# Performance work log

Hardware: AMD Instinct MI355X
Metric: run time of the kernel (lower is better)

The kernel has to match this reference:

```python
import jax, jax.numpy as jnp
import numpy as np

ALPHA = 0.2          # LeakyReLU negative slope
NEG_INF = -9e15      # mask value used by the original module


def setup_inputs() -> dict:
    key = jax.random.key(0)
    k1, k2, k3, k4 = jax.random.split(key, 4)
    N, C, F, H, E = 4096, 512, 64, 8, 131072
    x = jax.random.normal(k1, (N, C), dtype=jnp.float32)
    edge_index = jax.random.randint(k2, (2, E), 0, N, dtype=jnp.int64)
    # xavier_uniform with gain=1.414 (per-head params stacked on leading axis)
    lim_W = 1.414 * np.sqrt(6.0 / (C + F))
    lim_a = 1.414 * np.sqrt(6.0 / (2 * F + 1))
    W = jax.random.uniform(k3, (H, C, F), minval=-lim_W, maxval=lim_W, dtype=jnp.float32)
    a = jax.random.uniform(k4, (H, 2 * F, 1), minval=-lim_a, maxval=lim_a, dtype=jnp.float32)
    return {"x": x, "edge_index": edge_index, "W": W, "a": a}


def reference(x, edge_index, W, a):
    # x: [N, C]; edge_index: [2, E]; W: [H, C, F]; a: [H, 2F, 1]
    N = x.shape[0]
    H, C, F = W.shape
    # dense adjacency with self-loops (duplicate edges collapse to True, matching adj > 0)
    adj = jnp.zeros((N, N), dtype=bool).at[edge_index[0], edge_index[1]].set(True)
    diag = jnp.arange(N)
    adj = adj.at[diag, diag].set(True)
    # per-head projection: h[h_, i] = x_i @ W[h_]
    h = jnp.einsum('nc,hcf->hnf', x, W)                       # [H, N, F]
    # e_ij = leakyrelu(h_i . a[:F] + h_j . a[F:]) -- identical math to the
    # original's NxN pairwise concat, without materializing [N*N, 2F]
    a_src = a[:, :F, 0]                                        # [H, F]
    a_dst = a[:, F:, 0]                                        # [H, F]
    s_src = jnp.einsum('hnf,hf->hn', h, a_src)                 # [H, N]
    s_dst = jnp.einsum('hnf,hf->hn', h, a_dst)                 # [H, N]
    e = s_src[:, :, None] + s_dst[:, None, :]                  # [H, N, N]
    e = jnp.where(e > 0, e, ALPHA * e)                         # LeakyReLU
    e = jnp.where(adj[None, :, :], e, NEG_INF)                 # mask non-edges
    att = jax.nn.softmax(e, axis=-1)                           # row softmax (dropout=0 / eval)
    out = jnp.einsum('hij,hjf->hif', att, h)                   # [H, N, F]
    out = jnp.transpose(out, (1, 0, 2)).reshape(N, H * F)      # concat heads
    return jax.nn.softmax(out, axis=1)
```

## Files before the change

### kernel.cpp

```cpp
#include <hip/hip_runtime.h>

#define ALPHA 0.2f

typedef __attribute__((ext_vector_type(8))) short short8;
typedef __attribute__((ext_vector_type(8))) unsigned short ushort8;
typedef __attribute__((ext_vector_type(4))) float f32x4;

__device__ __forceinline__ float bf2f(unsigned short u) {
    return __uint_as_float(((unsigned int)u) << 16);
}
__device__ __forceinline__ unsigned short f2bf(float f) {
    unsigned int x = __float_as_uint(f);
    unsigned int r = (x + 0x7fffu + ((x >> 16) & 1u)) >> 16;
    return (unsigned short)r;
}

__global__ __launch_bounds__(256) void detect_types(const unsigned int* __restrict__ xw,
                                                    const int* __restrict__ ei32,
                                                    int* __restrict__ flags) {
    __shared__ int cnt[2];
    if (threadIdx.x == 0) { cnt[0] = 0; cnt[1] = 0; }
    __syncthreads();
    int c0 = 0, c1 = 0;
    int t = threadIdx.x;
    for (int i = 0; i < 8; i++) {
        int k = t * 8 + i;
        unsigned int u = xw[k];
        unsigned int e = (u >> 7) & 0xffu;
        if (e >= 0x58u && e <= 0x90u) c0++;
        if (ei32[2 * k + 1] != 0) c1++;
    }
    atomicAdd(&cnt[0], c0);
    atomicAdd(&cnt[1], c1);
    __syncthreads();
    if (threadIdx.x == 0) {
        flags[0] = (cnt[0] < 1200) ? 1 : 0;
        flags[1] = (cnt[1] < 1000) ? 1 : 0;
    }
}

__global__ __launch_bounds__(256) void split_bf16(const void* __restrict__ x_raw,
                                                  const void* __restrict__ W_raw,
                                                  unsigned short* __restrict__ x_hi,
                                                  unsigned short* __restrict__ x_lo,
                                                  unsigned short* __restrict__ wt_hi,
                                                  unsigned short* __restrict__ wt_lo,
                                                  const int* __restrict__ flags) {
    int is32 = flags[0];
    int bid = blockIdx.x, tid = threadIdx.x;
    if (bid < 1024) {
        size_t base = ((size_t)bid * 256 + tid) * 8;
        ushort8 h8, l8;
        if (is32) {
            const float* xf = (const float*)x_raw;
            float4 v0 = *(const float4*)(xf + base);
            float4 v1 = *(const float4*)(xf + base + 4);
            float v[8] = {v0.x, v0.y, v0.z, v0.w, v1.x, v1.y, v1.z, v1.w};
#pragma unroll
            for (int j = 0; j < 8; j++) {
                unsigned short hi = f2bf(v[j]);
                h8[j] = hi;
                l8[j] = f2bf(v[j] - bf2f(hi));
            }
        } else {
            const ushort8* xb = (const ushort8*)x_raw;
            h8 = xb[base / 8];
            l8 = (ushort8)0;
        }
        *(ushort8*)(x_hi + base) = h8;
        *(ushort8*)(x_lo + base) = l8;
    } else {
        size_t u = ((size_t)(bid - 1024) * 256 + tid) * 8;
#pragma unroll
        for (int j = 0; j < 8; j++) {
            size_t e = u + j;
            int head = (int)(e >> 15);
            int c = (int)((e >> 6) & 511);
            int f = (int)(e & 63);
            unsigned short hi, lo;
            if (is32) {
                float v = ((const float*)W_raw)[e];
                hi = f2bf(v);
                lo = f2bf(v - bf2f(hi));
            } else {
                hi = ((const unsigned short*)W_raw)[e];
                lo = 0;
            }
            size_t o = (size_t)head * 32768 + (size_t)f * 512 + c;
            wt_hi[o] = hi;
            wt_lo[o] = lo;
        }
    }
}

__global__ __launch_bounds__(256) void build_adj(const int* __restrict__ ei, int E, int N,
                                                 unsigned long long* __restrict__ adj,
                                                 const int* __restrict__ flags) {
    int is64 = flags[1];
    int t = blockIdx.x * blockDim.x + threadIdx.x;
    int words = N >> 6;
    if (t < E) {
        int r = is64 ? ei[2 * t]       : ei[t];
        int c = is64 ? ei[2 * (E + t)] : ei[E + t];
        atomicOr(&adj[(size_t)r * words + (c >> 6)], 1ull << (c & 63));
    } else if (t < E + N) {
        int i = t - E;
        atomicOr(&adj[(size_t)i * words + (i >> 6)], 1ull << (i & 63));
    }
}

#define LROW 40
__global__ __launch_bounds__(256) void gemm_mfma(const unsigned short* __restrict__ xh,
                                                 const unsigned short* __restrict__ xl,
                                                 const unsigned short* __restrict__ wth,
                                                 const unsigned short* __restrict__ wtl,
                                                 const void* __restrict__ a_raw,
                                                 unsigned short* __restrict__ h2b,
                                                 float* __restrict__ s_src2,
                                                 float* __restrict__ s_dst2,
                                                 const int* __restrict__ flags) {
    __shared__ unsigned short sA[64 * LROW];
    __shared__ unsigned short sB[64 * LROW];

    int head = blockIdx.y;
    int row0 = blockIdx.x * 64;
    int tid = threadIdx.x;
    int w = tid >> 6, lane = tid & 63;
    int m = lane & 15, quad = lane >> 4;
    int sr = tid >> 2, sc = tid & 3;

    const unsigned short* Ap[3] = {xh, xl, xh};
    const unsigned short* Bp[3] = {wth, wth, wtl};
    size_t baseA = (size_t)(row0 + sr) * 512 + sc * 8;
    size_t baseB = (size_t)head * 32768 + (size_t)sr * 512 + sc * 8;

    f32x4 acc[4] = {f32x4{0.f, 0.f, 0.f, 0.f}, f32x4{0.f, 0.f, 0.f, 0.f},
                    f32x4{0.f, 0.f, 0.f, 0.f}, f32x4{0.f, 0.f, 0.f, 0.f}};

    int ldsw = sr * LROW + sc * 8;
    int ldsA = (w * 16 + m) * LROW + quad * 8;

    ushort8 ra0 = *(const ushort8*)(Ap[0] + baseA);
    ushort8 rb0 = *(const ushort8*)(Bp[0] + baseB);
    ushort8 ra1 = *(const ushort8*)(Ap[0] + baseA + 32);
    ushort8 rb1 = *(const ushort8*)(Bp[0] + baseB + 32);

    for (int i = 0; i < 48; i += 2) {
        __syncthreads();
        *(ushort8*)&sA[ldsw] = ra0;
        *(ushort8*)&sB[ldsw] = rb0;
        __syncthreads();
        {
            int inx = i + 2;
            if (inx < 48) {
                int pn = inx >> 4, kn = (inx & 15) * 32;
                ra0 = *(const ushort8*)(Ap[pn] + baseA + kn);
                rb0 = *(const ushort8*)(Bp[pn] + baseB + kn);
            }
        }
        {
            short8 af = *(const short8*)&sA[ldsA];
#pragma unroll
            for (int t = 0; t < 4; t++) {
                short8 bf = *(const short8*)&sB[(t * 16 + m) * LROW + quad * 8];
                acc[t] = __builtin_amdgcn_mfma_f32_16x16x32_bf16(af, bf, acc[t], 0, 0, 0);
            }
        }
        __syncthreads();
        *(ushort8*)&sA[ldsw] = ra1;
        *(ushort8*)&sB[ldsw] = rb1;
        __syncthreads();
        {
            int inx = i + 3;
            if (inx < 48) {
                int pn = inx >> 4, kn = (inx & 15) * 32;
                ra1 = *(const ushort8*)(Ap[pn] + baseA + kn);
                rb1 = *(const ushort8*)(Bp[pn] + baseB + kn);
            }
        }
        {
            short8 af = *(const short8*)&sA[ldsA];
#pragma unroll
            for (int t = 0; t < 4; t++) {
                short8 bf = *(const short8*)&sB[(t * 16 + m) * LROW + quad * 8];
                acc[t] = __builtin_amdgcn_mfma_f32_16x16x32_bf16(af, bf, acc[t], 0, 0, 0);
            }
        }
    }

#pragma unroll
    for (int t = 0; t < 4; t++)
#pragma unroll
        for (int reg = 0; reg < 4; reg++) {
            int r = row0 + w * 16 + quad * 4 + reg;
            h2b[(size_t)r * 512 + head * 64 + t * 16 + m] = f2bf(acc[t][reg]);
        }

    float as[4], ad[4];
    if (flags[0]) {
        const float* af32 = (const float*)a_raw + head * 128;
#pragma unroll
        for (int t = 0; t < 4; t++) {
            as[t] = af32[t * 16 + m];
            ad[t] = af32[64 + t * 16 + m];
        }
    } else {
        const unsigned short* ab = (const unsigned short*)a_raw + head * 128;
#pragma unroll
        for (int t = 0; t < 4; t++) {
            as[t] = bf2f(ab[t * 16 + m]);
            ad[t] = bf2f(ab[64 + t * 16 + m]);
        }
    }
#pragma unroll
    for (int reg = 0; reg < 4; reg++) {
        float s1 = as[0] * acc[0][reg] + as[1] * acc[1][reg] + as[2] * acc[2][reg] + as[3] * acc[3][reg];
        float s2 = ad[0] * acc[0][reg] + ad[1] * acc[1][reg] + ad[2] * acc[2][reg] + ad[3] * acc[3][reg];
#pragma unroll
        for (int d = 1; d < 16; d <<= 1) {
            s1 += __shfl_xor(s1, d);
            s2 += __shfl_xor(s2, d);
        }
        if (m == 0) {
            int r = row0 + w * 16 + quad * 4 + reg;
            s_src2[(size_t)r * 8 + head] = s1;
            s_dst2[(size_t)r * 8 + head] = s2;
        }
    }
}

__global__ __launch_bounds__(256) void attn_out(const unsigned short* __restrict__ h2b,
                                                const float* __restrict__ s_src2,
                                                const float* __restrict__ s_dst2,
                                                const unsigned long long* __restrict__ adj,
                                                void* __restrict__ out_raw,
                                                const int* __restrict__ flags) {
    __shared__ unsigned short nbrs[4096];
    __shared__ float w_lds[256 * 8];
    __shared__ float sss[8], smax[8], sden[8];
    __shared__ float sredw[4][8];
    __shared__ float sr[8];
    __shared__ int s_cnt;

    int i = blockIdx.x;
    int tid = threadIdx.x;
    int lane = tid & 63, wid = tid >> 6;

    if (tid < 64) {
        unsigned long long word = adj[(size_t)i * 64 + tid];
        int cnt = __popcll(word);
        int incl = cnt;
#pragma unroll
        for (int d = 1; d < 64; d <<= 1) {
            int v = __shfl_up(incl, d);
            if (tid >= d) incl += v;
        }
        int off = incl - cnt;
        unsigned long long w = word;
        int base = tid * 64;
        while (w) {
            int b = __ffsll((unsigned long long)w) - 1;
            nbrs[off++] = (unsigned short)(base + b);
            w &= w - 1;
        }
        if (tid == 63) s_cnt = incl;
    }
    if (tid >= 64 && tid < 72) sss[tid - 64] = s_src2[(size_t)i * 8 + (tid - 64)];
    __syncthreads();
    int cnt = s_cnt;

    int hw = tid & 7;
    float mp = -1e30f;
    for (int t = tid; t < cnt * 8; t += 256)
        mp = fmaxf(mp, s_dst2[(size_t)nbrs[t >> 3] * 8 + hw]);
    mp = fmaxf(mp, __shfl_down(mp, 32));
    mp = fmaxf(mp, __shfl_down(mp, 16));
    mp = fmaxf(mp, __shfl_down(mp, 8));
    if (lane < 8) sredw[wid][lane] = mp;
    __syncthreads();
    if (tid < 8) {
        float m = fmaxf(fmaxf(sredw[0][tid], sredw[1][tid]), fmaxf(sredw[2][tid], sredw[3][tid]));
        float pre = sss[tid] + m;
        smax[tid] = pre > 0.f ? pre : ALPHA * pre;
    }
    __syncthreads();

    int hh = tid >> 5;
    float ssrc_w = sss[hw], maxe_w = smax[hw];
    float den = 0.f, ax = 0.f, ay = 0.f;
    for (int c0 = 0; c0 < cnt; c0 += 256) {
        int csz = min(256, cnt - c0);
        __syncthreads();
        for (int t = tid; t < csz * 8; t += 256) {
            int j = nbrs[c0 + (t >> 3)];
            float e = ssrc_w + s_dst2[(size_t)j * 8 + hw];
            e = e > 0.f ? e : ALPHA * e;
            float w = __expf(e - maxe_w);
            w_lds[t] = w;
            den += w;
        }
        __syncthreads();
#pragma unroll 2
        for (int jj = 0; jj < csz; jj++) {
            int j = nbrs[c0 + jj];
            unsigned int u = *(const unsigned int*)(h2b + (size_t)j * 512 + tid * 2);
            float w = w_lds[jj * 8 + hh];
            ax += w * bf2f((unsigned short)(u & 0xffffu));
            ay += w * bf2f((unsigned short)(u >> 16));
        }
    }

    den += __shfl_down(den, 32);
    den += __shfl_down(den, 16);
    den += __shfl_down(den, 8);
    if (lane < 8) sredw[wid][lane] = den;
    __syncthreads();
    if (tid < 8) sden[tid] = sredw[0][tid] + sredw[1][tid] + sredw[2][tid] + sredw[3][tid];
    __syncthreads();
    float dtot = sden[hh];
    float o0 = ax / dtot, o1 = ay / dtot;

    float m2 = fmaxf(o0, o1);
#pragma unroll
    for (int d = 32; d; d >>= 1) m2 = fmaxf(m2, __shfl_down(m2, d));
    if (lane == 0) sr[wid] = m2;
    __syncthreads();
    float m = fmaxf(fmaxf(sr[0], sr[1]), fmaxf(sr[2], sr[3]));
    float e0 = __expf(o0 - m), e1 = __expf(o1 - m);
    float s = e0 + e1;
#pragma unroll
    for (int d = 32; d; d >>= 1) s += __shfl_down(s, d);
    __syncthreads();
    if (lane == 0) sr[wid + 4] = s;
    __syncthreads();
    s = sr[4] + sr[5] + sr[6] + sr[7];

    if (flags[0]) {
        float2* out = (float2*)out_raw;
        out[(size_t)i * 256 + tid] = make_float2(e0 / s, e1 / s);
    } else {
        unsigned int* out = (unsigned int*)out_raw;
        out[(size_t)i * 256 + tid] = (unsigned int)f2bf(e0 / s) | ((unsigned int)f2bf(e1 / s) << 16);
    }
}

extern "C" void kernel_launch(void* const* d_in, const int* in_sizes, int n_in,
                              void* d_out, int out_size, void* d_ws, size_t ws_size,
                              hipStream_t stream) {
    const int N = 4096, H = 8;
    const int E = in_sizes[1] / 2;

    const void* x = d_in[0];
    const int*  ei = (const int*)d_in[1];
    const void* W = d_in[2];
    const void* a = d_in[3];

    char* ws = (char*)d_ws;
    unsigned short* h2b = (unsigned short*)ws;
    float* s_src2 = (float*)(ws + (size_t)4 * 1024 * 1024);
    float* s_dst2 = s_src2 + (size_t)N * H;
    unsigned long long* adj = (unsigned long long*)(ws + (size_t)5 * 1024 * 1024);
    int* flags = (int*)(ws + (size_t)7 * 1024 * 1024 + 512 * 1024);
    unsigned short* x_hi  = (unsigned short*)(ws + (size_t)8 * 1024 * 1024);
    unsigned short* x_lo  = (unsigned short*)(ws + (size_t)12 * 1024 * 1024);
    unsigned short* wt_hi = (unsigned short*)(ws + (size_t)16 * 1024 * 1024);
    unsigned short* wt_lo = (unsigned short*)(ws + (size_t)16 * 1024 * 1024 + 512 * 1024);

    hipMemsetAsync(adj, 0, (size_t)N * (N / 8), stream);

    detect_types<<<1, 256, 0, stream>>>((const unsigned int*)x, ei, flags);
    split_bf16<<<1152, 256, 0, stream>>>(x, W, x_hi, x_lo, wt_hi, wt_lo, flags);
    build_adj<<<(E + N + 255) / 256, 256, 0, stream>>>(ei, E, N, adj, flags);
    gemm_mfma<<<dim3(N / 64, H), 256, 0, stream>>>(x_hi, x_lo, wt_hi, wt_lo, a,
                                                   h2b, s_src2, s_dst2, flags);
    attn_out<<<N, 256, 0, stream>>>(h2b, s_src2, s_dst2, adj, d_out, flags);
}
```

Baseline: 130.2 us.

## Inline dtype detection and double-buffer the GEMM LDS with wider K steps

Removes the separate detect_types launch by detecting input dtypes inside split_bf16 and build_adj with wave ballots. The GEMM moves to double-buffered LDS with 64-wide K chunks, which halves the barrier count and overlaps global loads with MFMA work. The cost is more LDS per block. The detection heuristics now sample fewer elements, so they are less robust.

Result: faster. 118.7 us, median of 2 (-8.9%).

```diff
diff --git a/kernel.cpp b/kernel.cpp
--- a/kernel.cpp
+++ b/kernel.cpp
@@ -15,28 +15,12 @@
     return (unsigned short)r;
 }
 
-__global__ __launch_bounds__(256) void detect_types(const unsigned int* __restrict__ xw,
-                                                    const int* __restrict__ ei32,
-                                                    int* __restrict__ flags) {
-    __shared__ int cnt[2];
-    if (threadIdx.x == 0) { cnt[0] = 0; cnt[1] = 0; }
-    __syncthreads();
-    int c0 = 0, c1 = 0;
-    int t = threadIdx.x;
-    for (int i = 0; i < 8; i++) {
-        int k = t * 8 + i;
-        unsigned int u = xw[k];
-        unsigned int e = (u >> 7) & 0xffu;
-        if (e >= 0x58u && e <= 0x90u) c0++;
-        if (ei32[2 * k + 1] != 0) c1++;
-    }
-    atomicAdd(&cnt[0], c0);
-    atomicAdd(&cnt[1], c1);
-    __syncthreads();
-    if (threadIdx.x == 0) {
-        flags[0] = (cnt[0] < 1200) ? 1 : 0;
-        flags[1] = (cnt[1] < 1000) ? 1 : 0;
-    }
+__device__ __forceinline__ int detect_is32(const unsigned int* xw) {
+    int lane = threadIdx.x & 63;
+    unsigned int u = xw[lane];
+    unsigned int e = (u >> 7) & 0xffu;
+    unsigned long long b = __ballot(e >= 0x58u && e <= 0x90u);
+    return (__popcll(b) < 40) ? 1 : 0;
 }
 
 __global__ __launch_bounds__(256) void split_bf16(const void* __restrict__ x_raw,
@@ -45,9 +29,11 @@
                                                   unsigned short* __restrict__ x_lo,
                                                   unsigned short* __restrict__ wt_hi,
                                                   unsigned short* __restrict__ wt_lo,
-                                                  const int* __restrict__ flags) {
-    int is32 = flags[0];
+                                                  int* __restrict__ flags) {
     int bid = blockIdx.x, tid = threadIdx.x;
+    int is32 = detect_is32((const unsigned int*)x_raw);
+    if (bid == 0 && tid == 0) flags[0] = is32;
+
     if (bid < 1024) {
         size_t base = ((size_t)bid * 256 + tid) * 8;
         ushort8 h8, l8;
@@ -94,9 +80,11 @@
 }
 
 __global__ __launch_bounds__(256) void build_adj(const int* __restrict__ ei, int E, int N,
-                                                 unsigned long long* __restrict__ adj,
-                                                 const int* __restrict__ flags) {
-    int is64 = flags[1];
+                                                 unsigned long long* __restrict__ adj) {
+    int lane = threadIdx.x & 63;
+    unsigned long long nz = __ballot(ei[2 * lane + 1] != 0);
+    int is64 = (nz == 0ull) ? 1 : 0;
+
     int t = blockIdx.x * blockDim.x + threadIdx.x;
     int words = N >> 6;
     if (t < E) {
@@ -109,7 +97,7 @@
     }
 }
 
-#define LROW 40
+#define LROW 72
 __global__ __launch_bounds__(256) void gemm_mfma(const unsigned short* __restrict__ xh,
                                                  const unsigned short* __restrict__ xl,
                                                  const unsigned short* __restrict__ wth,
@@ -119,73 +107,77 @@
                                                  float* __restrict__ s_src2,
                                                  float* __restrict__ s_dst2,
                                                  const int* __restrict__ flags) {
-    __shared__ unsigned short sA[64 * LROW];
-    __shared__ unsigned short sB[64 * LROW];
+    __shared__ unsigned short sA[2][64 * LROW];
+    __shared__ unsigned short sB[2][64 * LROW];
 
     int head = blockIdx.y;
     int row0 = blockIdx.x * 64;
     int tid = threadIdx.x;
     int w = tid >> 6, lane = tid & 63;
     int m = lane & 15, quad = lane >> 4;
-    int sr = tid >> 2, sc = tid & 3;
+    int srow = tid >> 2, sc = tid & 3;
 
     const unsigned short* Ap[3] = {xh, xl, xh};
     const unsigned short* Bp[3] = {wth, wth, wtl};
-    size_t baseA = (size_t)(row0 + sr) * 512 + sc * 8;
-    size_t baseB = (size_t)head * 32768 + (size_t)sr * 512 + sc * 8;
+    size_t baseA = (size_t)(row0 + srow) * 512 + sc * 8;
+    size_t baseB = (size_t)head * 32768 + (size_t)srow * 512 + sc * 8;
+
+    int ldsw  = srow * LROW + sc * 8;
+    int ldsAr = (w * 16 + m) * LROW + quad * 8;
 
     f32x4 acc[4] = {f32x4{0.f, 0.f, 0.f, 0.f}, f32x4{0.f, 0.f, 0.f, 0.f},
                     f32x4{0.f, 0.f, 0.f, 0.f}, f32x4{0.f, 0.f, 0.f, 0.f}};
 
-    int ldsw = sr * LROW + sc * 8;
-    int ldsA = (w * 16 + m) * LROW + quad * 8;
-
-    ushort8 ra0 = *(const ushort8*)(Ap[0] + baseA);
-    ushort8 rb0 = *(const ushort8*)(Bp[0] + baseB);
-    ushort8 ra1 = *(const ushort8*)(Ap[0] + baseA + 32);
-    ushort8 rb1 = *(const ushort8*)(Bp[0] + baseB + 32);
-
-    for (int i = 0; i < 48; i += 2) {
+#define LOADSET(Aa, Ab, Ba, Bb, c)                                         \
+    {                                                                      \
+        const unsigned short* pA = Ap[(c) >> 3];                           \
+        const unsigned short* pB = Bp[(c) >> 3];                           \
+        size_t ko = (size_t)((c) & 7) * 64;                                \
+        Aa = *(const ushort8*)(pA + baseA + ko);                           \
+        Ab = *(const ushort8*)(pA + baseA + ko + 32);                      \
+        Ba = *(const ushort8*)(pB + baseB + ko);                           \
+        Bb = *(const ushort8*)(pB + baseB + ko + 32);                      \
+    }
+
+#define WRITESET(buf, Aa, Ab, Ba, Bb)                                      \
+    {                                                                      \
+        *(ushort8*)&sA[buf][ldsw]      = Aa;                               \
+        *(ushort8*)&sA[buf][ldsw + 32] = Ab;                               \
+        *(ushort8*)&sB[buf][ldsw]      = Ba;                               \
+        *(ushort8*)&sB[buf][ldsw + 32] = Bb;                               \
+    }
+
+#define COMPUTE(buf)                                                       \
+    {                                                                      \
+        short8 af0 = *(const short8*)&sA[buf][ldsAr];                      \
+        short8 af1 = *(const short8*)&sA[buf][ldsAr + 32];                 \
+        _Pragma("unroll")                                                  \
+        for (int t = 0; t < 4; t++) {                                      \
+            int bo = (t * 16 + m) * LROW + quad * 8;                       \
+            short8 bf0 = *(const short8*)&sB[buf][bo];                     \
+            short8 bf1 = *(const short8*)&sB[buf][bo + 32];                \
+            acc[t] = __builtin_amdgcn_mfma_f32_16x16x32_bf16(af0, bf0, acc[t], 0, 0, 0); \
+            acc[t] = __builtin_amdgcn_mfma_f32_16x16x32_bf16(af1, bf1, acc[t], 0, 0, 0); \
+        }                                                                  \
+    }
+
+    ushort8 a0a, a0b, b0a, b0b;
+    ushort8 a1a, a1b, b1a, b1b;
+
+    LOADSET(a0a, a0b, b0a, b0b, 0)
+    LOADSET(a1a, a1b, b1a, b1b, 1)
+    WRITESET(0, a0a, a0b, b0a, b0b)
+    __syncthreads();
+
+    for (int i = 0; i < 24; i += 2) {
+        if (i + 2 < 24) LOADSET(a0a, a0b, b0a, b0b, i + 2)
+        COMPUTE(0)
+        WRITESET(1, a1a, a1b, b1a, b1b)
         __syncthreads();
-        *(ushort8*)&sA[ldsw] = ra0;
-        *(ushort8*)&sB[ldsw] = rb0;
+        if (i + 3 < 24) LOADSET(a1a, a1b, b1a, b1b, i + 3)
+        COMPUTE(1)
+        if (i + 2 < 24) WRITESET(0, a0a, a0b, b0a, b0b)
         __syncthreads();
-        {
-            int inx = i + 2;
-            if (inx < 48) {
-                int pn = inx >> 4, kn = (inx & 15) * 32;
-                ra0 = *(const ushort8*)(Ap[pn] + baseA + kn);
-                rb0 = *(const ushort8*)(Bp[pn] + baseB + kn);
-            }
-        }
-        {
-            short8 af = *(const short8*)&sA[ldsA];
-#pragma unroll
-            for (int t = 0; t < 4; t++) {
-                short8 bf = *(const short8*)&sB[(t * 16 + m) * LROW + quad * 8];
-                acc[t] = __builtin_amdgcn_mfma_f32_16x16x32_bf16(af, bf, acc[t], 0, 0, 0);
-            }
-        }
-        __syncthreads();
-        *(ushort8*)&sA[ldsw] = ra1;
-        *(ushort8*)&sB[ldsw] = rb1;
-        __syncthreads();
-        {
-            int inx = i + 3;
-            if (inx < 48) {
-                int pn = inx >> 4, kn = (inx & 15) * 32;
-                ra1 = *(const ushort8*)(Ap[pn] + baseA + kn);
-                rb1 = *(const ushort8*)(Bp[pn] + baseB + kn);
-            }
-        }
-        {
-            short8 af = *(const short8*)&sA[ldsA];
-#pragma unroll
-            for (int t = 0; t < 4; t++) {
-                short8 bf = *(const short8*)&sB[(t * 16 + m) * LROW + quad * 8];
-                acc[t] = __builtin_amdgcn_mfma_f32_16x16x32_bf16(af, bf, acc[t], 0, 0, 0);
-            }
-        }
     }
 
 #pragma unroll
@@ -368,9 +360,8 @@
 
     hipMemsetAsync(adj, 0, (size_t)N * (N / 8), stream);
 
-    detect_types<<<1, 256, 0, stream>>>((const unsigned int*)x, ei, flags);
     split_bf16<<<1152, 256, 0, stream>>>(x, W, x_hi, x_lo, wt_hi, wt_lo, flags);
-    build_adj<<<(E + N + 255) / 256, 256, 0, stream>>>(ei, E, N, adj, flags);
+    build_adj<<<(E + N + 255) / 256, 256, 0, stream>>>(ei, E, N, adj);
     gemm_mfma<<<dim3(N / 64, H), 256, 0, stream>>>(x_hi, x_lo, wt_hi, wt_lo, a,
                                                    h2b, s_src2, s_dst2, flags);
     attn_out<<<N, 256, 0, stream>>>(h2b, s_src2, s_dst2, adj, d_out, flags);
```
